# Performance work log

Measured on AMD Instinct MI355X. Metric: run time of the kernel, lower is better.

Reference implementation:

```python
import jax, jax.numpy as jnp
import numpy as np
import math

B, SQ, SK, D = 32, 2048, 2048, 128


def setup_inputs() -> dict:
    key = jax.random.key(0)
    kq, kk, kv = jax.random.split(key, 3)
    queries = jax.random.normal(kq, (B, SQ, D), dtype=jnp.float32)
    keys = jax.random.normal(kk, (B, SK, D), dtype=jnp.float32)
    values = jax.random.normal(kv, (B, SK, D), dtype=jnp.float32)
    # causal mask: True = masked (future positions), broadcast over batch
    causal = jnp.triu(jnp.ones((SQ, SK), dtype=bool), k=1)
    mask = jnp.broadcast_to(causal, (B, SQ, SK))
    return {"queries": queries, "keys": keys, "values": values, "mask": mask}


def reference(queries, keys, values, mask):
    d = queries.shape[-1]
    scale = 1.0 / math.sqrt(d)
    # [B, Sq, Sk] score matrix (the module materializes this explicitly)
    scores = jnp.einsum("bqd,bkd->bqk", queries, keys) * scale
    scores = jnp.where(mask, -jnp.inf, scores)
    attn = jax.nn.softmax(scores, axis=-1)
    # dropout p=0.0 -> identity (eval parity)
    return jnp.einsum("bqk,bkd->bqd", attn, values)
```

## Files before the change

### kernel.cpp

```cpp
#include <hip/hip_runtime.h>
#include <hip/hip_bf16.h>

#define NB   32
#define SQL  2048
#define DH   128
#define QBLK 128
#define KBLK 64
#define NKT  (SQL / KBLK)
#define TILEB 16384

typedef __attribute__((ext_vector_type(4)))  float f32x4;
typedef __attribute__((ext_vector_type(16))) float f32x16;
typedef __attribute__((ext_vector_type(8)))  short s16x8;
typedef __attribute__((ext_vector_type(4)))  unsigned int u32x4;

__device__ __forceinline__ unsigned int cvtpk_bf16(float lo, float hi) {
  unsigned int r;
  asm("v_cvt_pk_bf16_f32 %0, %1, %2" : "=v"(r) : "v"(lo), "v"(hi));
  return r;
}
#define PLSWAP(x, y) asm volatile("v_permlane32_swap_b32 %0, %1" : "+v"(x), "+v"(y))

__device__ __forceinline__ unsigned int pk2(float lo, float hi) {
  unsigned short a = __builtin_bit_cast(unsigned short, __float2bfloat16(lo));
  unsigned short b = __builtin_bit_cast(unsigned short, __float2bfloat16(hi));
  return (unsigned int)a | ((unsigned int)b << 16);
}

#define AS1(p) ((const __attribute__((address_space(1))) void*)(p))
#define AS3(p) ((__attribute__((address_space(3))) void*)(p))

__global__ __launch_bounds__(256)
void prep_kv(const float* __restrict__ Kg, const float* __restrict__ Vg,
             char* __restrict__ wsK, char* __restrict__ wsV) {
  const int blk = blockIdx.x;
  const int b   = blk >> 5;
  const int kt  = blk & 31;
  const int tid = threadIdx.x;
  const float* Ksrc = Kg + ((size_t)b * SQL + (size_t)kt * KBLK) * DH;
  const float* Vsrc = Vg + ((size_t)b * SQL + (size_t)kt * KBLK) * DH;
  char* Kdst = wsK + (size_t)blk * TILEB;
  char* Vdst = wsV + (size_t)blk * TILEB;

  {
    const int q16 = tid & 15;
    const int r0  = tid >> 4;
    #pragma unroll
    for (int it = 0; it < 4; ++it) {
      const int r = r0 + 16 * it;
      const float* src = Ksrc + (size_t)r * DH + 8 * q16;
      f32x4 a = *(const f32x4*)(src);
      f32x4 d = *(const f32x4*)(src + 4);
      u32x4 w;
      w[0] = pk2(a[0], a[1]); w[1] = pk2(a[2], a[3]);
      w[2] = pk2(d[0], d[1]); w[3] = pk2(d[2], d[3]);
      *(u32x4*)(Kdst + ((r * 256 + 16 * q16) ^ ((r & 7) << 4))) = w;
    }
  }
  {
    const int kq = tid & 15;
    const int dq = tid >> 4;
    #pragma unroll
    for (int it = 0; it < 2; ++it) {
      const int d0 = 4 * dq + 64 * it;
      f32x4 rv[4];
      #pragma unroll
      for (int j = 0; j < 4; ++j)
        rv[j] = *(const f32x4*)(Vsrc + (size_t)(4 * kq + j) * DH + d0);
      #pragma unroll
      for (int j2 = 0; j2 < 4; ++j2) {
        const int dd = d0 + j2;
        uint2 w = make_uint2(pk2(rv[0][j2], rv[1][j2]), pk2(rv[2][j2], rv[3][j2]));
        *(uint2*)(Vdst + ((dd * 128 + 8 * kq) ^ ((dd & 7) << 4))) = w;
      }
    }
  }
}

__global__ __launch_bounds__(256, 2)
void attn_fwd(const float* __restrict__ Qg, const char* __restrict__ wsK,
              const char* __restrict__ wsV, float* __restrict__ Og) {
  __shared__ __align__(16) char smem[65536];

  const int tid  = threadIdx.x;
  const int wid  = tid >> 6;
  const int lane = tid & 63;
  const int hi   = lane >> 5;
  const int c    = lane & 31;

  const int i    = blockIdx.x;
  const int half = i >> 8;
  const int j    = i & 255;
  const int b    = j & 31;
  const int q3   = j >> 5;
  const int qt   = half ? (15 - q3) : q3;
  const int qb   = qt * QBLK;
  const int nt   = 2 * qt + 2;

  const float* Qb = Qg + (size_t)b * SQL * DH;
  float* Ob = Og + (size_t)b * SQL * DH;
  const char* Ktiles = wsK + (size_t)b * NKT * TILEB;
  const char* Vtiles = wsV + (size_t)b * NKT * TILEB;

  const float qscale = 0.08838834764831845f * 1.4426950408889634f;

  s16x8 qf[8];
  {
    const float* qr = Qb + (size_t)(qb + 32*wid + c) * DH + 8*hi;
    #pragma unroll
    for (int ds = 0; ds < 8; ++ds) {
      f32x4 a = *(const f32x4*)(qr + 16*ds);
      f32x4 d = *(const f32x4*)(qr + 16*ds + 4);
      u32x4 w;
      w[0] = pk2(a[0]*qscale, a[1]*qscale);
      w[1] = pk2(a[2]*qscale, a[3]*qscale);
      w[2] = pk2(d[0]*qscale, d[1]*qscale);
      w[3] = pk2(d[2]*qscale, d[3]*qscale);
      qf[ds] = __builtin_bit_cast(s16x8, w);
    }
  }

  f32x16 oacc[4];
  #pragma unroll
  for (int nb = 0; nb < 4; ++nb) oacc[nb] = (f32x16){0.f};
  float m_run = -1e30f, l_run = 0.f;

  const int qglob = qb + 32*wid + c;
  const int qhiw  = qb + 32*wid + 31;
  const int qlow  = qb + 32*wid;

  auto STAGE = [&](int t) {
    const char* ks = Ktiles + (size_t)t * TILEB + tid * 16;
    const char* vs = Vtiles + (size_t)t * TILEB + tid * 16;
    char* kl = smem + (t & 1) * 16384 + wid * 1024;
    char* vl = smem + 32768 + (t & 1) * 16384 + wid * 1024;
    #pragma unroll
    for (int jj = 0; jj < 4; ++jj) {
      __builtin_amdgcn_global_load_lds(AS1(ks + jj * 4096), AS3(kl + jj * 4096), 16, 0, 0);
      __builtin_amdgcn_global_load_lds(AS1(vs + jj * 4096), AS3(vl + jj * 4096), 16, 0, 0);
    }
  };

  STAGE(0);
  STAGE(1);

  for (int t = 0; t < nt; ++t) {
    if (t == nt - 1) asm volatile("s_waitcnt vmcnt(0)" ::: "memory");
    else             asm volatile("s_waitcnt vmcnt(8)" ::: "memory");
    __builtin_amdgcn_s_barrier();
    __builtin_amdgcn_sched_barrier(0);

    const int kb = t * KBLK;
    const char* Kl = smem + (t & 1) * 16384;
    const char* Vl = smem + 32768 + (t & 1) * 16384;

    if (kb <= qhiw) {
      f32x16 sacc[2];
      sacc[0] = (f32x16){0.f};
      sacc[1] = (f32x16){0.f};
      __builtin_amdgcn_s_setprio(1);
      #pragma unroll
      for (int ds = 0; ds < 8; ++ds) {
        #pragma unroll
        for (int mb = 0; mb < 2; ++mb) {
          const int row = 32*mb + c;
          s16x8 kf = *(const s16x8*)(Kl + ((row*256 + 32*ds + 16*hi) ^ ((c & 7) << 4)));
          sacc[mb] = __builtin_amdgcn_mfma_f32_32x32x16_bf16(kf, qf[ds], sacc[mb], 0, 0, 0);
        }
      }
      __builtin_amdgcn_s_setprio(0);

      if (kb + KBLK - 1 > qlow) {
        #pragma unroll
        for (int mb = 0; mb < 2; ++mb)
          #pragma unroll
          for (int r = 0; r < 16; ++r) {
            const int kk = kb + 32*mb + (r & 3) + 8*(r >> 2) + 4*hi;
            if (kk > qglob) sacc[mb][r] = -1e30f;
          }
      }

      float mx[8];
      #pragma unroll
      for (int e = 0; e < 8; ++e)
        mx[e] = fmaxf(fmaxf(sacc[0][e], sacc[0][e+8]), fmaxf(sacc[1][e], sacc[1][e+8]));
      mx[0] = fmaxf(mx[0], mx[4]); mx[1] = fmaxf(mx[1], mx[5]);
      mx[2] = fmaxf(mx[2], mx[6]); mx[3] = fmaxf(mx[3], mx[7]);
      const float tmax = fmaxf(fmaxf(mx[0], mx[1]), fmaxf(mx[2], mx[3]));

      if (!__all(tmax <= m_run + 8.0f)) {
        float tfull = fmaxf(tmax, __shfl_xor(tmax, 32));
        const float mnew  = fmaxf(m_run, tfull);
        const float alpha = exp2f(m_run - mnew);
        #pragma unroll
        for (int r = 0; r < 16; ++r) {
          float av = __shfl(alpha, (r & 3) + 8*(r >> 2) + 4*hi);
          #pragma unroll
          for (int nb = 0; nb < 4; ++nb) oacc[nb][r] *= av;
        }
        l_run *= alpha;
        m_run = mnew;
      }

      float lsa = 0.f, lsb = 0.f;
      unsigned int u0[8], u1[8];
      #pragma unroll
      for (int w = 0; w < 8; ++w) {
        float p0 = exp2f(sacc[0][2*w]     - m_run);
        float p1 = exp2f(sacc[0][2*w + 1] - m_run);
        lsa += p0 + p1;
        u0[w] = cvtpk_bf16(p0, p1);
      }
      #pragma unroll
      for (int w = 0; w < 8; ++w) {
        float p0 = exp2f(sacc[1][2*w]     - m_run);
        float p1 = exp2f(sacc[1][2*w + 1] - m_run);
        lsb += p0 + p1;
        u1[w] = cvtpk_bf16(p0, p1);
      }
      l_run += lsa + lsb;

      PLSWAP(u0[0], u0[2]); PLSWAP(u0[1], u0[3]);
      PLSWAP(u0[4], u0[6]); PLSWAP(u0[5], u0[7]);
      PLSWAP(u1[0], u1[2]); PLSWAP(u1[1], u1[3]);
      PLSWAP(u1[4], u1[6]); PLSWAP(u1[5], u1[7]);
      s16x8 pa[4];
      { u32x4 w = {u0[0], u0[1], u0[2], u0[3]}; pa[0] = __builtin_bit_cast(s16x8, w); }
      { u32x4 w = {u0[4], u0[5], u0[6], u0[7]}; pa[1] = __builtin_bit_cast(s16x8, w); }
      { u32x4 w = {u1[0], u1[1], u1[2], u1[3]}; pa[2] = __builtin_bit_cast(s16x8, w); }
      { u32x4 w = {u1[4], u1[5], u1[6], u1[7]}; pa[3] = __builtin_bit_cast(s16x8, w); }

      __builtin_amdgcn_s_setprio(1);
      #pragma unroll
      for (int nb = 0; nb < 4; ++nb) {
        #pragma unroll
        for (int ks = 0; ks < 4; ++ks) {
          const int row = 32*nb + c;
          s16x8 vf = *(const s16x8*)(Vl + ((row*128 + 32*ks + 16*hi) ^ ((c & 7) << 4)));
          oacc[nb] = __builtin_amdgcn_mfma_f32_32x32x16_bf16(pa[ks], vf, oacc[nb], 0, 0, 0);
        }
      }
      __builtin_amdgcn_s_setprio(0);
    }

    __builtin_amdgcn_s_barrier();
    if (t + 2 < nt) STAGE(t + 2);
  }

  const float l_tot = l_run + __shfl_xor(l_run, 32);
  const float linv  = 1.0f / l_tot;
  float* Orow = Ob + (size_t)(qb + 32*wid) * DH;
  #pragma unroll
  for (int r = 0; r < 16; ++r) {
    const int q = (r & 3) + 8*(r >> 2) + 4*hi;
    float lv = __shfl(linv, q);
    #pragma unroll
    for (int nb = 0; nb < 4; ++nb)
      Orow[(size_t)q * DH + 32*nb + c] = oacc[nb][r] * lv;
  }
}

extern "C" void kernel_launch(void* const* d_in, const int* in_sizes, int n_in,
                              void* d_out, int out_size, void* d_ws, size_t ws_size,
                              hipStream_t stream) {
  const float* Q = (const float*)d_in[0];
  const float* K = (const float*)d_in[1];
  const float* V = (const float*)d_in[2];
  float* O = (float*)d_out;
  char* wsK = (char*)d_ws;
  char* wsV = (char*)d_ws + (size_t)NB * NKT * TILEB;

  prep_kv<<<dim3(NB * NKT), dim3(256), 0, stream>>>(K, V, wsK, wsV);
  attn_fwd<<<dim3(NB * (SQL / QBLK)), dim3(256), 0, stream>>>(Q, wsK, wsV, O);
}
```

Baseline: 86.72 us.

## Load V fragments directly from global memory and halve LDS footprint

```diff
diff --git a/kernel.cpp b/kernel.cpp
--- a/kernel.cpp
+++ b/kernel.cpp
@@ -80,7 +80,7 @@
 __global__ __launch_bounds__(256, 2)
 void attn_fwd(const float* __restrict__ Qg, const char* __restrict__ wsK,
               const char* __restrict__ wsV, float* __restrict__ Og) {
-  __shared__ __align__(16) char smem[65536];
+  __shared__ __align__(16) char smem[32768];
 
   const int tid  = threadIdx.x;
   const int wid  = tid >> 6;
@@ -89,11 +89,11 @@
   const int c    = lane & 31;
 
   const int i    = blockIdx.x;
-  const int half = i >> 8;
-  const int j    = i & 255;
-  const int b    = j & 31;
-  const int q3   = j >> 5;
-  const int qt   = half ? (15 - q3) : q3;
+  const int x    = i & 7;
+  const int j    = i >> 3;
+  const int b    = x + 8 * (j & 3);
+  const int qrow = j >> 2;
+  const int qt   = (qrow < 8) ? qrow : (23 - qrow);
   const int qb   = qt * QBLK;
   const int nt   = 2 * qt + 2;
 
@@ -131,14 +131,10 @@
 
   auto STAGE = [&](int t) {
     const char* ks = Ktiles + (size_t)t * TILEB + tid * 16;
-    const char* vs = Vtiles + (size_t)t * TILEB + tid * 16;
     char* kl = smem + (t & 1) * 16384 + wid * 1024;
-    char* vl = smem + 32768 + (t & 1) * 16384 + wid * 1024;
-    #pragma unroll
-    for (int jj = 0; jj < 4; ++jj) {
+    #pragma unroll
+    for (int jj = 0; jj < 4; ++jj)
       __builtin_amdgcn_global_load_lds(AS1(ks + jj * 4096), AS3(kl + jj * 4096), 16, 0, 0);
-      __builtin_amdgcn_global_load_lds(AS1(vs + jj * 4096), AS3(vl + jj * 4096), 16, 0, 0);
-    }
   };
 
   STAGE(0);
@@ -146,13 +142,13 @@
 
   for (int t = 0; t < nt; ++t) {
     if (t == nt - 1) asm volatile("s_waitcnt vmcnt(0)" ::: "memory");
-    else             asm volatile("s_waitcnt vmcnt(8)" ::: "memory");
+    else             asm volatile("s_waitcnt vmcnt(4)" ::: "memory");
     __builtin_amdgcn_s_barrier();
     __builtin_amdgcn_sched_barrier(0);
 
     const int kb = t * KBLK;
-    const char* Kl = smem + (t & 1) * 16384;
-    const char* Vl = smem + 32768 + (t & 1) * 16384;
+    const char* Kl  = smem + (t & 1) * 16384;
+    const char* Vgt = Vtiles + (size_t)t * TILEB;
 
     if (kb <= qhiw) {
       f32x16 sacc[2];
@@ -169,6 +165,14 @@
         }
       }
       __builtin_amdgcn_s_setprio(0);
+
+      s16x8 vka[4], vkb[4];
+      #pragma unroll
+      for (int nb = 0; nb < 4; ++nb) {
+        const int row = 32*nb + c;
+        vka[nb] = *(const s16x8*)(Vgt + ((row*128 +  0 + 16*hi) ^ ((c & 7) << 4)));
+        vkb[nb] = *(const s16x8*)(Vgt + ((row*128 + 32 + 16*hi) ^ ((c & 7) << 4)));
+      }
 
       if (kb + KBLK - 1 > qlow) {
         #pragma unroll
@@ -220,6 +224,14 @@
       }
       l_run += lsa + lsb;
 
+      s16x8 vkc[4], vkd[4];
+      #pragma unroll
+      for (int nb = 0; nb < 4; ++nb) {
+        const int row = 32*nb + c;
+        vkc[nb] = *(const s16x8*)(Vgt + ((row*128 + 64 + 16*hi) ^ ((c & 7) << 4)));
+        vkd[nb] = *(const s16x8*)(Vgt + ((row*128 + 96 + 16*hi) ^ ((c & 7) << 4)));
+      }
+
       PLSWAP(u0[0], u0[2]); PLSWAP(u0[1], u0[3]);
       PLSWAP(u0[4], u0[6]); PLSWAP(u0[5], u0[7]);
       PLSWAP(u1[0], u1[2]); PLSWAP(u1[1], u1[3]);
@@ -232,14 +244,17 @@
 
       __builtin_amdgcn_s_setprio(1);
       #pragma unroll
-      for (int nb = 0; nb < 4; ++nb) {
-        #pragma unroll
-        for (int ks = 0; ks < 4; ++ks) {
-          const int row = 32*nb + c;
-          s16x8 vf = *(const s16x8*)(Vl + ((row*128 + 32*ks + 16*hi) ^ ((c & 7) << 4)));
-          oacc[nb] = __builtin_amdgcn_mfma_f32_32x32x16_bf16(pa[ks], vf, oacc[nb], 0, 0, 0);
-        }
-      }
+      for (int nb = 0; nb < 4; ++nb)
+        oacc[nb] = __builtin_amdgcn_mfma_f32_32x32x16_bf16(pa[0], vka[nb], oacc[nb], 0, 0, 0);
+      #pragma unroll
+      for (int nb = 0; nb < 4; ++nb)
+        oacc[nb] = __builtin_amdgcn_mfma_f32_32x32x16_bf16(pa[1], vkb[nb], oacc[nb], 0, 0, 0);
+      #pragma unroll
+      for (int nb = 0; nb < 4; ++nb)
+        oacc[nb] = __builtin_amdgcn_mfma_f32_32x32x16_bf16(pa[2], vkc[nb], oacc[nb], 0, 0, 0);
+      #pragma unroll
+      for (int nb = 0; nb < 4; ++nb)
+        oacc[nb] = __builtin_amdgcn_mfma_f32_32x32x16_bf16(pa[3], vkd[nb], oacc[nb], 0, 0, 0);
       __builtin_amdgcn_s_setprio(0);
     }
 
```

Result: slower. 97.31 us (+12.2%).
